# Performance work log

Measured on AMD Instinct MI355X. Metric: run time of the kernel, lower is better.

Reference implementation:

```python
import jax, jax.numpy as jnp
import numpy as np

M, NC, NT, DX = 8, 1024, 512, 3
CHUNK = 512          # chunk_size
N_STEPS = 8          # n_steps (tol=0.0 -> torch early-stop never fires)
LR = 0.1
B1, B2, EPS = 0.9, 0.999, 1e-8
SQRT5 = 5.0 ** 0.5
LOG2PI = float(np.log(2.0 * np.pi))
NOISE_LB = 1e-4      # gpytorch GreaterThan(1e-4) noise constraint


def setup_inputs():
    key = jax.random.key(0)
    k1, k2, k3 = jax.random.split(key, 3)
    return {
        "xc": jax.random.normal(k1, (M, NC, DX), jnp.float32),
        "yc": jax.random.normal(k2, (M, NC, 1), jnp.float32),
        "xt": jax.random.normal(k3, (M, NT, DX), jnp.float32),
    }


def _kernel(x1, x2, ls, outscale):
    # ScaleKernel(MaternKernel(nu=2.5)); ls: [m,1,1], outscale: [m]
    xs1, xs2 = x1 / ls, x2 / ls
    d2 = (jnp.sum(xs1 * xs1, -1)[:, :, None]
          + jnp.sum(xs2 * xs2, -1)[:, None, :]
          - 2.0 * jnp.einsum('mnd,mkd->mnk', xs1, xs2))
    d2 = jnp.clip(d2, 1e-12, None)   # clamp like gpytorch dist for grad safety
    d = jnp.sqrt(d2)
    k = (1.0 + SQRT5 * d + (5.0 / 3.0) * d2) * jnp.exp(-SQRT5 * d)
    return outscale[:, None, None] * k


def _constrained(params):
    ls = jax.nn.softplus(params["raw_ls"])                          # [m,1,1]
    outscale = jax.nn.softplus(params["raw_os"])                    # [m]
    noise = jax.nn.softplus(params["raw_noise"][:, 0]) + NOISE_LB   # [m]
    return ls, outscale, noise


def _nll(params, x, y):
    # sum over tasks of -ExactMarginalLogLikelihood (gpytorch divides by n)
    ls, outscale, noise = _constrained(params)
    n = x.shape[1]
    K = _kernel(x, x, ls, outscale) + noise[:, None, None] * jnp.eye(n, dtype=x.dtype)
    L = jnp.linalg.cholesky(K)
    diff = y - params["const"][:, None]
    alpha = jax.scipy.linalg.cho_solve((L, True), diff[..., None])[..., 0]
    quad = jnp.sum(diff * alpha, -1)
    logdet = 2.0 * jnp.sum(jnp.log(jnp.diagonal(L, axis1=-2, axis2=-1)), -1)
    mll = -0.5 * (quad + logdet + n * LOG2PI) / n
    return jnp.sum(-mll)


def _adam_step(carry, x_sub, y_sub):
    p, m_, v_, t = carry
    g = jax.grad(_nll)(p, x_sub, y_sub)
    t = t + 1.0
    tm = jax.tree_util.tree_map
    m_ = tm(lambda a, gg: B1 * a + (1.0 - B1) * gg, m_, g)
    v_ = tm(lambda a, gg: B2 * a + (1.0 - B2) * gg * gg, v_, g)
    bc1 = 1.0 - B1 ** t
    bc2 = 1.0 - B2 ** t
    p = tm(lambda pp, mm, vv: pp - LR * (mm / bc1) / (jnp.sqrt(vv / bc2) + EPS), p, m_, v_)
    return (p, m_, v_, t)


def _gp_forward(xc, yc, xt):
    y = yc[..., 0]                                    # [m, nc]
    zl = lambda s: jnp.zeros(s, jnp.float32)
    # gpytorch raw params initialize to 0
    params = {"raw_ls": zl((M, 1, 1)), "raw_os": zl((M,)),
              "raw_noise": zl((M, 1)), "const": zl((M,))}
    m_ = jax.tree_util.tree_map(jnp.zeros_like, params)
    v_ = jax.tree_util.tree_map(jnp.zeros_like, params)
    carry = (params, m_, v_, jnp.float32(0.0))
    for i in range(0, NC, CHUNK):                     # 'Expanding' strategy
        end = min(i + CHUNK, NC)
        x_sub, y_sub = xc[:, :end], y[:, :end]
        step = lambda c, _: (_adam_step(c, x_sub, y_sub), None)
        carry, _ = jax.lax.scan(step, carry, None, length=N_STEPS)
    params = carry[0]
    # posterior predictive with trained hypers (train data = full context)
    ls, outscale, noise = _constrained(params)
    Kcc = _kernel(xc, xc, ls, outscale) + noise[:, None, None] * jnp.eye(NC, dtype=xc.dtype)
    L = jnp.linalg.cholesky(Kcc)
    diff = y - params["const"][:, None]
    alpha = jax.scipy.linalg.cho_solve((L, True), diff[..., None])[..., 0]
    Ktc = _kernel(xt, xc, ls, outscale)               # [m, nt, nc]
    mean = params["const"][:, None] + jnp.einsum('mtn,mn->mt', Ktc, alpha)
    v = jax.scipy.linalg.solve_triangular(L, jnp.swapaxes(Ktc, 1, 2), lower=True)  # [m,nc,nt]
    var_f = outscale[:, None] - jnp.sum(v * v, axis=1)  # Matern(0)=1 -> prior diag = outputscale
    var = var_f + noise[:, None]                      # likelihood(f) adds observation noise
    return jnp.stack([mean, var])                     # [2, m, nt]


def reference(xc, yc, xt):
    return _gp_forward(xc, yc, xt)
```

## Files before the change

kernel.cpp:

```cpp
#include <hip/hip_runtime.h>
#include <math.h>

constexpr int MM = 8;
constexpr int NC = 1024;
constexpr int NT = 512;
constexpr int GRID = 512;
constexpr int GPB  = GRID / MM;

constexpr size_t OFF_A     = (size_t)MM * 1024 * 1024;
constexpr size_t OFF_T     = OFF_A * 2;
constexpr size_t OFF_KTC   = OFF_T + (size_t)MM * 512 * 512;
constexpr size_t OFF_ALPHA = OFF_KTC + (size_t)MM * NT * NC;
constexpr size_t OFF_ACC   = OFF_ALPHA + (size_t)MM * 1024;

#define S5 2.2360679775f

struct GBar {
  unsigned slot[GPB][16];
  unsigned gen[16];
  unsigned xcd[GPB][16];
};
__device__ GBar g_bar2[MM];

__device__ __forceinline__ unsigned bar_base(int m) {
  return __hip_atomic_load(&g_bar2[m].gen[0], __ATOMIC_RELAXED, __HIP_MEMORY_SCOPE_AGENT);
}

__device__ __forceinline__ void gbar_full(int m, int gb, unsigned ph) {
  __syncthreads();
  GBar* b = &g_bar2[m];
  const int tid = threadIdx.x;
  if (gb == 0) {
    if (tid >= 1 && tid < GPB) {
      while (__hip_atomic_load(&b->slot[tid][0], __ATOMIC_RELAXED, __HIP_MEMORY_SCOPE_AGENT) < ph)
        __builtin_amdgcn_s_sleep(2);
    }
    __syncthreads();
    if (tid == 0) {
      __threadfence();
      __hip_atomic_store(&b->gen[0], ph, __ATOMIC_RELAXED, __HIP_MEMORY_SCOPE_AGENT);
    }
    __syncthreads();
  } else {
    if (tid == 0) {
      __threadfence();
      __hip_atomic_store(&b->slot[gb][0], ph, __ATOMIC_RELAXED, __HIP_MEMORY_SCOPE_AGENT);
      while (__hip_atomic_load(&b->gen[0], __ATOMIC_RELAXED, __HIP_MEMORY_SCOPE_AGENT) < ph)
        __builtin_amdgcn_s_sleep(8);
      __threadfence();
    }
    __syncthreads();
  }
}

__device__ __forceinline__ void gbar_cheap(int m, int gb, unsigned ph) {
  __syncthreads();
  GBar* b = &g_bar2[m];
  const int tid = threadIdx.x;
  if (gb == 0) {
    if (tid >= 1 && tid < GPB) {
      while (__hip_atomic_load(&b->slot[tid][0], __ATOMIC_RELAXED, __HIP_MEMORY_SCOPE_AGENT) < ph)
        __builtin_amdgcn_s_sleep(2);
    }
    __syncthreads();
    if (tid == 0) {
      asm volatile("s_waitcnt vmcnt(0)" ::: "memory");
      __hip_atomic_store(&b->gen[0], ph, __ATOMIC_RELAXED, __HIP_MEMORY_SCOPE_AGENT);
    }
    __syncthreads();
  } else {
    if (tid == 0) {
      asm volatile("s_waitcnt vmcnt(0)" ::: "memory");
      __hip_atomic_store(&b->slot[gb][0], ph, __ATOMIC_RELAXED, __HIP_MEMORY_SCOPE_AGENT);
      while (__hip_atomic_load(&b->gen[0], __ATOMIC_RELAXED, __HIP_MEMORY_SCOPE_AGENT) < ph)
        __builtin_amdgcn_s_sleep(8);
    }
    __syncthreads();
  }
}

__device__ __forceinline__ void gbar(int m, int gb, unsigned& ph, int cheap) {
  if (cheap) gbar_cheap(m, gb, ph); else gbar_full(m, gb, ph);
  ph++;
}

__device__ __forceinline__ float sigmf(float x) { return 1.0f / (1.0f + expf(-x)); }
__device__ __forceinline__ float softplusf(float x) { return fmaxf(x, 0.0f) + log1pf(expf(-fabsf(x))); }

__device__ __forceinline__ void lt_decode(int x, int& i, int& j) {
  int ii = 0;
  while ((ii + 1) * (ii + 2) / 2 <= x) ++ii;
  i = ii; j = x - ii * (ii + 1) / 2;
}

struct SMem {
  float Ls[64 * 65];
  float Us[64 * 65];
  float Tt[32 * 33];
  float dvec[64];
  float As[16][68];
  float Bs[16][68];
  float xi[64][3];
  float xj[64][3];
  float ai[64];
  float aj[64];
  float red[4][4];
  unsigned bar0;
  int cheap;
};

template <int TA, int TB>
__device__ __forceinline__ void gemm64(const volatile float* __restrict__ A, int lda,
                                       const volatile float* __restrict__ B, int ldb,
                                       int kBeg, int kEnd, float acc[4][4], SMem& sm) {
  int tid = threadIdx.x, tx = tid & 15, ty = tid >> 4;
  float ra[4], rb[4];
  auto ldAB = [&](int k0) {
#pragma unroll
    for (int q = 0; q < 4; ++q) {
      int e = tid + (q << 8);
      if (TA) { int kk = e >> 6, r = e & 63; ra[q] = A[(size_t)(k0 + kk) * lda + r]; }
      else    { int r = e >> 4, kk = e & 15; ra[q] = A[(size_t)r * lda + k0 + kk]; }
      if (TB) { int c = e >> 4, kk = e & 15; rb[q] = B[(size_t)c * ldb + k0 + kk]; }
      else    { int kk = e >> 6, c = e & 63; rb[q] = B[(size_t)(k0 + kk) * ldb + c]; }
    }
  };
  ldAB(kBeg);
  for (int k0 = kBeg; k0 < kEnd; k0 += 16) {
    __syncthreads();
#pragma unroll
    for (int q = 0; q < 4; ++q) {
      int e = tid + (q << 8);
      if (TA) sm.As[e >> 6][e & 63] = ra[q]; else sm.As[e & 15][e >> 4] = ra[q];
      if (TB) sm.Bs[e & 15][e >> 4] = rb[q]; else sm.Bs[e >> 6][e & 63] = rb[q];
    }
    __syncthreads();
    if (k0 + 16 < kEnd) ldAB(k0 + 16);
#pragma unroll
    for (int kk = 0; kk < 16; ++kk) {
      float a[4], b[4];
#pragma unroll
      for (int i = 0; i < 4; ++i) a[i] = sm.As[kk][ty * 4 + i];
#pragma unroll
      for (int j = 0; j < 4; ++j) b[j] = sm.Bs[kk][tx * 4 + j];
#pragma unroll
      for (int i = 0; i < 4; ++i)
#pragma unroll
        for (int j = 0; j < 4; ++j) acc[i][j] = fmaf(a[i], b[j], acc[i][j]);
    }
  }
}

__device__ void factor64(SMem& sm, float* Uout, int ldu) {
  int tid = threadIdx.x;
  int tx = tid & 15, ty = tid >> 4;
  for (int j = 0; j < 63; ++j) {
    float rinv = 1.0f / sm.Ls[j * 65 + j];
    for (int i = j + 1 + ty; i < 64; i += 16) {
      float lij = sm.Ls[i * 65 + j] * rinv;
      for (int c = j + 1 + tx; c <= i; c += 16) sm.Ls[i * 65 + c] -= lij * sm.Ls[c * 65 + j];
    }
    __syncthreads();
  }
  if (tid < 64) sm.dvec[tid] = 1.0f / sqrtf(sm.Ls[tid * 65 + tid]);
  __syncthreads();
  for (int e = tid; e < 4096; e += 256) { int r = e >> 6, c = e & 63; if (c <= r) sm.Ls[r * 65 + c] *= sm.dvec[c]; }
  __syncthreads();
  for (int e = tid; e < 64 * 65; e += 256) sm.Us[e] = 0.0f;
  __syncthreads();
  if (tid < 64) {
    int b = tid >> 5, c0 = tid & 31, base = b * 32, gc = base + c0;
    sm.Us[gc * 65 + gc] = 1.0f / sm.Ls[gc * 65 + gc];
    for (int r = c0 + 1; r < 32; ++r) {
      int gr = base + r;
      float acc = 0.0f;
      for (int l = c0; l < r; ++l) acc += sm.Ls[gr * 65 + base + l] * sm.Us[(base + l) * 65 + gc];
      sm.Us[gr * 65 + gc] = -acc / sm.Ls[gr * 65 + gr];
    }
  }
  __syncthreads();
  for (int e = tid; e < 1024; e += 256) {
    int r = e >> 5, c = e & 31;
    float acc = 0.0f;
    for (int l = c; l < 32; ++l) acc += sm.Ls[(32 + r) * 65 + l] * sm.Us[l * 65 + c];
    sm.Tt[r * 33 + c] = acc;
  }
  __syncthreads();
  for (int e = tid; e < 1024; e += 256) {
    int r = e >> 5, c = e & 31;
    float acc = 0.0f;
    for (int l = 0; l <= r; ++l) acc += sm.Us[(32 + r) * 65 + 32 + l] * sm.Tt[l * 33 + c];
    sm.Us[(32 + r) * 65 + c] = -acc;
  }
  __syncthreads();
  for (int e = tid; e < 4096; e += 256) { int r = e >> 6, c = e & 63; Uout[(size_t)r * ldu + c] = sm.Us[r * 65 + c]; }
}


__device__ void adam_all(const float* __restrict__ yc, const float* __restrict__ ws,
                         int pn, int tstep, int m, int tid, SMem& sm,
                         float praw[4], float pm[4], float pv[4],
                         float& ls, float& os, float& noi, float& cm) {
  const volatile float* al = ws + OFF_ALPHA + (size_t)m * 1024;
  const volatile float* accp = ws + OFF_ACC + m * 8;
  const float* ym = yc + (size_t)m * NC;
  float t4 = 0, t5 = 0, t6 = 0;
  for (int i = tid; i < pn; i += 256) {
    float a = al[i];
    t4 = fmaf(a, a, t4); t5 += a; t6 = fmaf(ym[i] - cm, a, t6);
  }
  for (int off = 32; off; off >>= 1) {
    t4 += __shfl_down(t4, off); t5 += __shfl_down(t5, off); t6 += __shfl_down(t6, off);
  }
  int wid = tid >> 6, lane = tid & 63;
  if (lane == 0) { sm.red[wid][0] = t4; sm.red[wid][1] = t5; sm.red[wid][2] = t6; }
  __syncthreads();
  t4 = sm.red[0][0] + sm.red[1][0] + sm.red[2][0] + sm.red[3][0];
  t5 = sm.red[0][1] + sm.red[1][1] + sm.red[2][1] + sm.red[3][1];
  t6 = sm.red[0][2] + sm.red[1][2] + sm.red[2][2] + sm.red[3][2];
  float T1 = accp[0], T2 = accp[1], t3 = accp[2];
  float fn = (float)pn;
  float g_ls = 0.5f / fn * (T1 - T2);
  float g_os = 0.5f / (fn * os) * (fn - noi * t3 - t6 + noi * t4);
  float g_no = 0.5f / fn * (t3 - t4);
  float g_c = -t5 / fn;
  float gr[4];
  gr[0] = g_ls * sigmf(praw[0]);
  gr[1] = g_os * sigmf(praw[1]);
  gr[2] = g_no * sigmf(praw[2]);
  gr[3] = g_c;
  float bc1 = 1.0f - powf(0.9f, (float)tstep);
  float bc2 = 1.0f - powf(0.999f, (float)tstep);
#pragma unroll
  for (int i = 0; i < 4; ++i) {
    float mv = 0.9f * pm[i] + 0.1f * gr[i];
    float vv = 0.999f * pv[i] + 0.001f * gr[i] * gr[i];
    pm[i] = mv; pv[i] = vv;
    praw[i] = praw[i] - 0.1f * (mv / bc1) / (sqrtf(vv / bc2) + 1e-8f);
  }
  ls = softplusf(praw[0]);
  os = softplusf(praw[1]);
  noi = softplusf(praw[2]) + 1e-4f;
  cm = praw[3];
  __syncthreads();
}

__device__ void d_buildK(const float* __restrict__ xc, float* ws, int n, int job, int m,
                         int tid, SMem& sm, float ls, float os, float noi) {
  const float* xm = xc + (size_t)m * NC * 3;
  float* Km = ws + (size_t)m * 1048576;
  float* Am = ws + OFF_A + (size_t)m * 1048576;
  float il2 = 1.0f / (ls * ls);
  int bi, bj; lt_decode(job, bi, bj);
  if (tid < 64) {
    int r = bi * 64 + tid;
    sm.xi[tid][0] = xm[r * 3 + 0]; sm.xi[tid][1] = xm[r * 3 + 1]; sm.xi[tid][2] = xm[r * 3 + 2];
  } else if (tid < 128) {
    int lr = tid - 64; int r = bj * 64 + lr;
    sm.xj[lr][0] = xm[r * 3 + 0]; sm.xj[lr][1] = xm[r * 3 + 1]; sm.xj[lr][2] = xm[r * 3 + 2];
  }
  __syncthreads();
  if (job == 0) {
    for (int e = tid; e < 4096; e += 256) {
      int r = e >> 6, c = e & 63;
      float d0 = sm.xi[r][0] - sm.xj[c][0], d1 = sm.xi[r][1] - sm.xj[c][1], d2 = sm.xi[r][2] - sm.xj[c][2];
      float r2 = d0 * d0 + d1 * d1 + d2 * d2;
      float z = fmaxf(r2 * il2, 1e-12f);
      float dd = sqrtf(z);
      float kv = os * (1.0f + S5 * dd + (5.0f / 3.0f) * z) * expf(-S5 * dd);
      if (r == c) kv += noi;
      sm.Ls[r * 65 + c] = kv;
    }
    __syncthreads();
    factor64(sm, Am, n);
  } else {
    for (int e = tid; e < 4096; e += 256) {
      int r = e >> 6, c = e & 63;
      float d0 = sm.xi[r][0] - sm.xj[c][0], d1 = sm.xi[r][1] - sm.xj[c][1], d2 = sm.xi[r][2] - sm.xj[c][2];
      float r2 = d0 * d0 + d1 * d1 + d2 * d2;
      float z = fmaxf(r2 * il2, 1e-12f);
      float dd = sqrtf(z);
      float kv = os * (1.0f + S5 * dd + (5.0f / 3.0f) * z) * expf(-S5 * dd);
      if (bi == bj && r == c) kv += noi;
      Km[(size_t)(bi * 64 + r) * n + bj * 64 + c] = kv;
    }
  }
}

__device__ void d_trail(float* ws, int k, int n, int job, int m, int tid, SMem& sm) {
  int tx = tid & 15, ty = tid >> 4;
  float* Km = ws + (size_t)m * 1048576;
  float* Am = ws + OFF_A + (size_t)m * 1048576;
  const volatile float* Linv = Am + (size_t)(k * 64) * n + k * 64;
  int di, dj; lt_decode(job, di, dj);
  int i = k + 1 + di, j = k + 1 + dj;
  float pp[4][4] = {};
  gemm64<0, 1>(Km + (size_t)(i * 64) * n + k * 64, n, Linv, n, 0, 64, pp, sm);
  __syncthreads();
#pragma unroll
  for (int ii = 0; ii < 4; ++ii)
#pragma unroll
    for (int jj = 0; jj < 4; ++jj) sm.Ls[(ty * 4 + ii) * 65 + tx * 4 + jj] = pp[ii][jj];
  if (di == dj) {
    float* P = Am + (size_t)(i * 64) * n + k * 64;
#pragma unroll
    for (int ii = 0; ii < 4; ++ii)
#pragma unroll
      for (int jj = 0; jj < 4; ++jj) P[(size_t)(ty * 4 + ii) * n + tx * 4 + jj] = pp[ii][jj];
  } else {
#pragma unroll
    for (int ii = 0; ii < 4; ++ii)
#pragma unroll
      for (int jj = 0; jj < 4; ++jj) pp[ii][jj] = 0.0f;
    gemm64<0, 1>(Km + (size_t)(j * 64) * n + k * 64, n, Linv, n, 0, 64, pp, sm);
#pragma unroll
    for (int ii = 0; ii < 4; ++ii)
#pragma unroll
      for (int jj = 0; jj < 4; ++jj) sm.Us[(ty * 4 + ii) * 65 + tx * 4 + jj] = pp[ii][jj];
  }
  __syncthreads();
  float acc[4][4] = {};
  {
    const float* Bsrc = (di == dj) ? sm.Ls : sm.Us;
    for (int l = 0; l < 64; ++l) {
      float a[4], b[4];
#pragma unroll
      for (int ii = 0; ii < 4; ++ii) a[ii] = sm.Ls[(ty * 4 + ii) * 65 + l];
#pragma unroll
      for (int jj = 0; jj < 4; ++jj) b[jj] = Bsrc[(tx * 4 + jj) * 65 + l];
#pragma unroll
      for (int ii = 0; ii < 4; ++ii)
#pragma unroll
        for (int jj = 0; jj < 4; ++jj) acc[ii][jj] = fmaf(a[ii], b[jj], acc[ii][jj]);
    }
  }
  float* C = Km + (size_t)(i * 64) * n + j * 64;
  if (job == 0) {
    const volatile float* Cv = C;
    __syncthreads();
#pragma unroll
    for (int ii = 0; ii < 4; ++ii)
#pragma unroll
      for (int jj = 0; jj < 4; ++jj)
        sm.Ls[(ty * 4 + ii) * 65 + tx * 4 + jj] =
            Cv[(size_t)(ty * 4 + ii) * n + tx * 4 + jj] - acc[ii][jj];
    __syncthreads();
    factor64(sm, Am + (size_t)((k + 1) * 64) * n + (k + 1) * 64, n);
  } else {
    const volatile float* Cv = C;
#pragma unroll
    for (int ii = 0; ii < 4; ++ii)
#pragma unroll
      for (int jj = 0; jj < 4; ++jj)
        C[(size_t)(ty * 4 + ii) * n + tx * 4 + jj] =
            Cv[(size_t)(ty * 4 + ii) * n + tx * 4 + jj] - acc[ii][jj];
  }
}

__device__ void d_trinv64(float* ws, int n, int p, int m, int tid, SMem& sm) {
  int tx = tid & 15, ty = tid >> 4;
  float* Am = ws + OFF_A + (size_t)m * 1048576;
  const volatile float* Av = Am;
  int rb = (2 * p + 1) * 64, cb = 2 * p * 64;
  for (int e = tid; e < 4096; e += 256) {
    int r = e >> 6, c = e & 63;
    sm.Ls[r * 65 + c] = Av[(size_t)(rb + r) * n + cb + c];
    sm.Us[r * 65 + c] = Av[(size_t)(cb + r) * n + cb + c];
  }
  __syncthreads();
  float tt[4][4] = {};
  for (int l = 0; l < 64; ++l) {
    float a[4], b[4];
#pragma unroll
    for (int ii = 0; ii < 4; ++ii) a[ii] = sm.Ls[(ty * 4 + ii) * 65 + l];
#pragma unroll
    for (int jj = 0; jj < 4; ++jj) b[jj] = sm.Us[l * 65 + tx * 4 + jj];
#pragma unroll
    for (int ii = 0; ii < 4; ++ii)
#pragma unroll
      for (int jj = 0; jj < 4; ++jj) tt[ii][jj] = fmaf(a[ii], b[jj], tt[ii][jj]);
  }
  __syncthreads();
#pragma unroll
  for (int ii = 0; ii < 4; ++ii)
#pragma unroll
    for (int jj = 0; jj < 4; ++jj) sm.Ls[(ty * 4 + ii) * 65 + tx * 4 + jj] = tt[ii][jj];
  for (int e = tid; e < 4096; e += 256) {
    int r = e >> 6, c = e & 63;
    sm.Us[r * 65 + c] = Av[(size_t)(rb + r) * n + rb + c];
  }
  __syncthreads();
  float oo[4][4] = {};
  for (int l = 0; l < 64; ++l) {
    float a[4], b[4];
#pragma unroll
    for (int ii = 0; ii < 4; ++ii) a[ii] = sm.Us[(ty * 4 + ii) * 65 + l];
#pragma unroll
    for (int jj = 0; jj < 4; ++jj) b[jj] = sm.Ls[l * 65 + tx * 4 + jj];
#pragma unroll
    for (int ii = 0; ii < 4; ++ii)
#pragma unroll
      for (int jj = 0; jj < 4; ++jj) oo[ii][jj] = fmaf(a[ii], b[jj], oo[ii][jj]);
  }
#pragma unroll
  for (int ii = 0; ii < 4; ++ii)
#pragma unroll
    for (int jj = 0; jj < 4; ++jj)
      Am[(size_t)(rb + ty * 4 + ii) * n + cb + tx * 4 + jj] = -oo[ii][jj];
}

__device__ void d_trinvT(float* ws, int s, int n, int job, int m, int tid, SMem& sm) {
  int tx = tid & 15, ty = tid >> 4;
  float* Am = ws + OFF_A + (size_t)m * 1048576;
  float* Tm = ws + OFF_T + (size_t)m * 262144;
  int st = s >> 6;
  int p = job / (st * st), rem = job % (st * st);
  int ti = rem / st, tj = rem % st;
  int base = p * 2 * s;
  float acc[4][4] = {};
  gemm64<0, 0>(Am + (size_t)(base + s + ti * 64) * n + base, n,
               Am + (size_t)base * n + base + tj * 64, n, tj * 64, s, acc, sm);
  float* C = Tm + (size_t)p * s * s + (size_t)(ti * 64) * s + tj * 64;
#pragma unroll
  for (int ii = 0; ii < 4; ++ii)
#pragma unroll
    for (int jj = 0; jj < 4; ++jj) C[(size_t)(ty * 4 + ii) * s + tx * 4 + jj] = acc[ii][jj];
}

__device__ void d_trinvA(float* ws, int s, int n, int job, int m, int tid, SMem& sm) {
  int tx = tid & 15, ty = tid >> 4;
  float* Am = ws + OFF_A + (size_t)m * 1048576;
  const volatile float* Tm = ws + OFF_T + (size_t)m * 262144;
  int st = s >> 6;
  int p = job / (st * st), rem = job % (st * st);
  int ti = rem / st, tj = rem % st;
  int base = p * 2 * s;
  float acc[4][4] = {};
  gemm64<0, 0>(Am + (size_t)(base + s + ti * 64) * n + base + s, n,
               Tm + (size_t)p * s * s + tj * 64, s, 0, (ti + 1) * 64, acc, sm);
  float* C = Am + (size_t)(base + s + ti * 64) * n + base + tj * 64;
#pragma unroll
  for (int ii = 0; ii < 4; ++ii)
#pragma unroll
    for (int jj = 0; jj < 4; ++jj) C[(size_t)(ty * 4 + ii) * n + tx * 4 + jj] = -acc[ii][jj];
}

__device__ void d_syrkAT(const float* __restrict__ yc, const float* __restrict__ xc,
                         float* ws, int n, int job, int m, int tid, SMem& sm,
                         float cm, float ls, float os, bool writeG) {
  int tx = tid & 15, ty = tid >> 4;
  const float* Am = ws + OFF_A + (size_t)m * 1048576;
  float* Gm = ws + (size_t)m * 1048576;
  const float* ym = yc + (size_t)m * NC;
  const float* xm = xc + (size_t)m * NC * 3;
  float* accp = ws + OFF_ACC + m * 8;
  float* al = ws + OFF_ALPHA + (size_t)m * 1024;
  int ib, jb; lt_decode(job, ib, jb);
  if (tid < 64) {
    int r = ib * 64 + tid;
    sm.ai[tid] = ym[r] - cm;
    sm.xi[tid][0] = xm[r * 3 + 0]; sm.xi[tid][1] = xm[r * 3 + 1]; sm.xi[tid][2] = xm[r * 3 + 2];
  } else if (tid < 128) {
    int lr = tid - 64; int r = jb * 64 + lr;
    sm.aj[lr] = ym[r] - cm;
    sm.xj[lr][0] = xm[r * 3 + 0]; sm.xj[lr][1] = xm[r * 3 + 1]; sm.xj[lr][2] = xm[r * 3 + 2];
  }
  float acc[4][4] = {};
  gemm64<1, 0>(Am + ib * 64, n, Am + jb * 64, n, ib * 64, n, acc, sm);
  if (writeG) {
#pragma unroll
    for (int ii = 0; ii < 4; ++ii)
#pragma unroll
      for (int jj = 0; jj < 4; ++jj) {
        int r = ty * 4 + ii, c = tx * 4 + jj;
        Gm[(size_t)(ib * 64 + r) * n + jb * 64 + c] = acc[ii][jj];
        if (ib != jb) Gm[(size_t)(jb * 64 + c) * n + ib * 64 + r] = acc[ii][jj];
      }
  }
  if (ib == jb && tx == ty) {
    atomicAdd(&accp[2], acc[0][0] + acc[1][1] + acc[2][2] + acc[3][3]);
  }
  float rowp[4];
#pragma unroll
  for (int i = 0; i < 4; ++i) {
    float s = 0.0f;
#pragma unroll
    for (int j = 0; j < 4; ++j) s = fmaf(acc[i][j], sm.aj[tx * 4 + j], s);
    rowp[i] = s;
  }
  float colp[4];
  if (ib != jb) {
#pragma unroll
    for (int j = 0; j < 4; ++j) {
      float s = 0.0f;
#pragma unroll
      for (int i = 0; i < 4; ++i) s = fmaf(acc[i][j], sm.ai[ty * 4 + i], s);
      colp[j] = s;
    }
  }
  float il2 = 1.0f / (ls * ls);
  float c53 = (5.0f / 3.0f) * os / ls;
  float a1 = 0.0f;
#pragma unroll
  for (int ii = 0; ii < 4; ++ii) {
    int r = ty * 4 + ii;
#pragma unroll
    for (int jj = 0; jj < 4; ++jj) {
      int c = tx * 4 + jj;
      float d0 = sm.xi[r][0] - sm.xj[c][0], d1 = sm.xi[r][1] - sm.xj[c][1], d2 = sm.xi[r][2] - sm.xj[c][2];
      float r2 = d0 * d0 + d1 * d1 + d2 * d2;
      float z = fmaxf(r2 * il2, 1e-12f);
      float dd = sqrtf(z);
      float Cv = c53 * z * (1.0f + S5 * dd) * expf(-S5 * dd);
      a1 = fmaf(acc[ii][jj], Cv, a1);
    }
  }
  a1 *= (ib == jb) ? 1.0f : 2.0f;
  for (int off = 32; off; off >>= 1) a1 += __shfl_down(a1, off);
  int wid = tid >> 6, lane = tid & 63;
  if (lane == 0) sm.red[wid][0] = a1;
  __syncthreads();
  if (tid == 0)
    atomicAdd(&accp[0], sm.red[0][0] + sm.red[1][0] + sm.red[2][0] + sm.red[3][0]);
  float* redA = &sm.As[0][0];
  float* redB = &sm.Bs[0][0];
#pragma unroll
  for (int i = 0; i < 4; ++i) redA[(ty * 4 + i) * 16 + tx] = rowp[i];
  if (ib != jb) {
#pragma unroll
    for (int j = 0; j < 4; ++j) redB[(tx * 4 + j) * 16 + ty] = colp[j];
  }
  __syncthreads();
  if (tid < 64) {
    float s = 0.0f;
#pragma unroll
    for (int q = 0; q < 16; ++q) s += redA[tid * 16 + q];
    atomicAdd(&al[ib * 64 + tid], s);
    if (ib != jb) {
      float s2 = 0.0f;
#pragma unroll
      for (int q = 0; q < 16; ++q) s2 += redB[tid * 16 + q];
      atomicAdd(&al[jb * 64 + tid], s2);
    }
  }
}

__device__ void d_reduce2(const float* __restrict__ xc, float* ws, int n, int job, int m,
                          int tid, SMem& sm, float ls, float os) {
  const float* xm = xc + (size_t)m * NC * 3;
  const volatile float* al = ws + OFF_ALPHA + (size_t)m * 1024;
  float* accp = ws + OFF_ACC + m * 8;
  float il2 = 1.0f / (ls * ls);
  float c53 = (5.0f / 3.0f) * os / ls;
  int bi, bj; lt_decode(job, bi, bj);
  float w = (bi == bj) ? 1.0f : 2.0f;
  if (tid < 64) {
    int r = bi * 64 + tid;
    sm.xi[tid][0] = xm[r * 3 + 0]; sm.xi[tid][1] = xm[r * 3 + 1]; sm.xi[tid][2] = xm[r * 3 + 2];
    sm.ai[tid] = al[r];
  } else if (tid < 128) {
    int lr = tid - 64; int r = bj * 64 + lr;
    sm.xj[lr][0] = xm[r * 3 + 0]; sm.xj[lr][1] = xm[r * 3 + 1]; sm.xj[lr][2] = xm[r * 3 + 2];
    sm.aj[lr] = al[r];
  }
  __syncthreads();
  float a2 = 0.0f;
  for (int e = tid; e < 4096; e += 256) {
    int r = e >> 6, c = e & 63;
    float d0 = sm.xi[r][0] - sm.xj[c][0], d1 = sm.xi[r][1] - sm.xj[c][1], d2 = sm.xi[r][2] - sm.xj[c][2];
    float r2 = d0 * d0 + d1 * d1 + d2 * d2;
    float z = fmaxf(r2 * il2, 1e-12f);
    float dd = sqrtf(z);
    float Cv = c53 * z * (1.0f + S5 * dd) * expf(-S5 * dd);
    a2 = fmaf(sm.ai[r] * sm.aj[c], Cv, a2);
  }
  a2 *= w;
  for (int off = 32; off; off >>= 1) a2 += __shfl_down(a2, off);
  int wid = tid >> 6, lane = tid & 63;
  if (lane == 0) sm.red[wid][1] = a2;
  __syncthreads();
  if (tid == 0) {
    atomicAdd(&accp[1], sm.red[0][1] + sm.red[1][1] + sm.red[2][1] + sm.red[3][1]);
  }
}

__device__ void d_buildKtc(const float* __restrict__ xt, const float* __restrict__ xc,
                           float* ws, int job, int m, int tid, SMem& sm, float ls, float os) {
  const float* xtm = xt + (size_t)m * NT * 3;
  const float* xm = xc + (size_t)m * NC * 3;
  float* Kt = ws + OFF_KTC + (size_t)m * NT * NC;
  float* Tm = ws + OFF_T + (size_t)m * 262144;
  float il2 = 1.0f / (ls * ls);
  if (job < 2) {
    int z = job * 256 + tid;
    Tm[z] = 0.0f; Tm[NT + z] = 0.0f;
  }
  int ti = job >> 4, tj = job & 15;
  if (tid < 64) {
    int r = ti * 64 + tid;
    sm.xi[tid][0] = xtm[r * 3 + 0]; sm.xi[tid][1] = xtm[r * 3 + 1]; sm.xi[tid][2] = xtm[r * 3 + 2];
  } else if (tid < 128) {
    int lr = tid - 64; int r = tj * 64 + lr;
    sm.xj[lr][0] = xm[r * 3 + 0]; sm.xj[lr][1] = xm[r * 3 + 1]; sm.xj[lr][2] = xm[r * 3 + 2];
  }
  __syncthreads();
  for (int e = tid; e < 4096; e += 256) {
    int r = e >> 6, c = e & 63;
    float d0 = sm.xi[r][0] - sm.xj[c][0], d1 = sm.xi[r][1] - sm.xj[c][1], d2 = sm.xi[r][2] - sm.xj[c][2];
    float r2 = d0 * d0 + d1 * d1 + d2 * d2;
    float z = fmaxf(r2 * il2, 1e-12f);
    float dd = sqrtf(z);
    float kv = os * (1.0f + S5 * dd + (5.0f / 3.0f) * z) * expf(-S5 * dd);
    Kt[(size_t)(ti * 64 + r) * NC + tj * 64 + c] = kv;
  }
}

__device__ void d_predW(float* ws, int job, int m, int tid, SMem& sm) {
  int tx = tid & 15, ty = tid >> 4;
  const volatile float* Kt = ws + OFF_KTC + (size_t)m * NT * NC;
  const volatile float* Gm = ws + (size_t)m * 1048576;
  const volatile float* al = ws + OFF_ALPHA + (size_t)m * 1024;
  float* S1 = ws + OFF_T + (size_t)m * 262144;
  float* S2 = S1 + NT;
  int ti = job >> 4, tj = job & 15;
  if (tid < 64) sm.aj[tid] = al[tj * 64 + tid];
  float acc[4][4] = {};
  gemm64<0, 0>(Kt + (size_t)(ti * 64) * NC, NC, Gm + tj * 64, 1024, 0, 1024, acc, sm);
  float s1p[4], s2p[4];
#pragma unroll
  for (int i = 0; i < 4; ++i) {
    float a1 = 0.0f, a2 = 0.0f;
    const volatile float* kr = Kt + (size_t)(ti * 64 + ty * 4 + i) * NC + tj * 64;
#pragma unroll
    for (int j = 0; j < 4; ++j) {
      float kv = kr[tx * 4 + j];
      a1 = fmaf(kv, sm.aj[tx * 4 + j], a1);
      a2 = fmaf(kv, acc[i][j], a2);
    }
    s1p[i] = a1; s2p[i] = a2;
  }
  __syncthreads();
  float* redA = &sm.As[0][0];
  float* redB = &sm.Bs[0][0];
#pragma unroll
  for (int i = 0; i < 4; ++i) {
    redA[(ty * 4 + i) * 16 + tx] = s1p[i];
    redB[(ty * 4 + i) * 16 + tx] = s2p[i];
  }
  __syncthreads();
  if (tid < 64) {
    float a1 = 0.0f, a2 = 0.0f;
#pragma unroll
    for (int q = 0; q < 16; ++q) { a1 += redA[tid * 16 + q]; a2 += redB[tid * 16 + q]; }
    atomicAdd(&S1[ti * 64 + tid], a1);
    atomicAdd(&S2[ti * 64 + tid], a2);
  }
}

__global__ __launch_bounds__(256, 2) void k_gp(const float* __restrict__ xc,
                                               const float* __restrict__ yc,
                                               const float* __restrict__ xt,
                                               float* ws, float* out) {
  __shared__ SMem sm;
  const int bid = blockIdx.x;
  const int m  = bid % MM;
  const int gb = bid / MM;
  const int tid = threadIdx.x;

  if (tid == 0) sm.bar0 = bar_base(m);
  __syncthreads();
  unsigned ph = sm.bar0 + 1;

  if (tid == 0) {
    unsigned x;
    asm volatile("s_getreg_b32 %0, hwreg(HW_REG_XCC_ID)" : "=s"(x));
    __hip_atomic_store(&g_bar2[m].xcd[gb][0], x, __ATOMIC_RELAXED, __HIP_MEMORY_SCOPE_AGENT);
  }
  gbar_full(m, gb, ph);
  ph++;
  if (tid < GPB) {
    unsigned v = __hip_atomic_load(&g_bar2[m].xcd[tid][0], __ATOMIC_RELAXED, __HIP_MEMORY_SCOPE_AGENT);
    unsigned v0 = __shfl(v, 0, 64);
    unsigned long long bal = __ballot(v == v0);
    if (tid == 0) sm.cheap = (bal == ~0ull) ? 1 : 0;
  }
  __syncthreads();
  const int cheap = sm.cheap;

  float praw[4] = {0.f, 0.f, 0.f, 0.f};
  float pm[4]   = {0.f, 0.f, 0.f, 0.f};
  float pv[4]   = {0.f, 0.f, 0.f, 0.f};
  float ls = 0.69314718056f, os = 0.69314718056f;
  float noi = 0.69314718056f + 1e-4f, cm = 0.0f;

  for (int step = 0; step < 17; ++step) {
    const int n = step < 8 ? 512 : 1024;
    const int nb = n >> 6;
    const bool lastStep = (step == 16);

    if (step > 0) {
      adam_all(yc, ws, step <= 8 ? 512 : 1024, step, m, tid, sm,
               praw, pm, pv, ls, os, noi, cm);
    }
    {
      const int tot = nb * (nb + 1) / 2;
      if (gb == 0) {
        __syncthreads();
        d_buildK(xc, ws, n, 0, m, tid, sm, ls, os, noi);
      } else {
        for (int q = gb; q < tot; q += GPB - 1) {
          __syncthreads();
          d_buildK(xc, ws, n, q, m, tid, sm, ls, os, noi);
        }
      }
      gbar(m, gb, ph, cheap);
    }

    for (int k = 0; k <= nb - 2; ++k) {
      const int t = nb - 1 - k;
      const int tot = t * (t + 1) / 2;
      if (gb == 0) {
        if (k == 0) {
          float* al = ws + OFF_ALPHA + (size_t)m * 1024;
          for (int z = tid; z < 1024; z += 256) al[z] = 0.0f;
          if (tid < 8) ws[OFF_ACC + m * 8 + tid] = 0.0f;
        }
        __syncthreads();
        d_trail(ws, k, n, 0, m, tid, sm);
      } else {
        for (int q = gb; q < tot; q += GPB - 1) {
          __syncthreads();
          d_trail(ws, k, n, q, m, tid, sm);
        }
        if ((k & 1) && gb == GPB - 1) {
          __syncthreads();
          d_trinv64(ws, n, k >> 1, m, tid, sm);
        }
      }
      gbar(m, gb, ph, cheap);
    }

    for (int s = 128; s < n; s <<= 1) {
      const int st = s >> 6;
      const int np = n / (2 * s);
      const int tot = np * st * st;
      for (int q = gb; q < tot; q += GPB) {
        __syncthreads();
        d_trinvT(ws, s, n, q, m, tid, sm);
      }
      if (s == 128 && gb == GPB - 1) {
        __syncthreads();
        d_trinv64(ws, n, nb / 2 - 1, m, tid, sm);
      }
      gbar(m, gb, ph, cheap);
      for (int q = gb; q < tot; q += GPB) {
        __syncthreads();
        d_trinvA(ws, s, n, q, m, tid, sm);
      }
      gbar(m, gb, ph, cheap);
    }

    {
      const int tot = nb * (nb + 1) / 2;
      for (int q = gb; q < tot; q += GPB) {
        __syncthreads();
        d_syrkAT(yc, xc, ws, n, q, m, tid, sm, cm, ls, os, lastStep);
      }
      gbar(m, gb, ph, cheap);
    }

    if (step < 16) {
      const int tot = nb * (nb + 1) / 2;
      for (int q = gb; q < tot; q += GPB) {
        __syncthreads();
        d_reduce2(xc, ws, n, q, m, tid, sm, ls, os);
      }
      gbar(m, gb, ph, cheap);
    }
  }

  {
    for (int q = gb; q < 128; q += GPB) {
      __syncthreads();
      d_buildKtc(xt, xc, ws, q, m, tid, sm, ls, os);
    }
    gbar(m, gb, ph, cheap);
    for (int q = gb; q < 128; q += GPB) {
      __syncthreads();
      d_predW(ws, q, m, tid, sm);
    }
    gbar(m, gb, ph, cheap);
    const volatile float* S1 = ws + OFF_T + (size_t)m * 262144;
    const volatile float* S2 = S1 + NT;
    for (int t = gb * 256 + tid; t < NT; t += GPB * 256) {
      out[(size_t)m * NT + t] = cm + S1[t];
      out[(size_t)MM * NT + (size_t)m * NT + t] = os + noi - S2[t];
    }
  }
}

extern "C" void kernel_launch(void* const* d_in, const int* in_sizes, int n_in,
                              void* d_out, int out_size, void* d_ws, size_t ws_size,
                              hipStream_t stream) {
  const float* xc = (const float*)d_in[0];
  const float* yc = (const float*)d_in[1];
  const float* xt = (const float*)d_in[2];
  float* out = (float*)d_out;
  float* ws = (float*)d_ws;

  hipLaunchKernelGGL(k_gp, dim3(GRID), dim3(256), 0, stream, xc, yc, xt, ws, out);

  (void)in_sizes; (void)n_in; (void)out_size; (void)ws_size;
}
```

Measured before the change: 21.46 ms.

## Map each task's block group to one XCD and use cheap intra-XCD barriers

Blocks now claim a rank within their hardware XCD at startup, so each of the 8 tasks runs entirely on one XCD with a variable group size. This lets every per-task barrier use the cheap waitcnt-only path instead of full device fences and lets shared data stay in one XCD's L2. It also raises wave priority for the critical-path block 0 work and serpentine-orders the syrk tile assignment for load balance. The risk is that XCD block counts are uneven, or that correctness now depends on the claim protocol and on all blocks being co-resident.

```diff
diff --git a/kernel.cpp b/kernel.cpp
--- a/kernel.cpp
+++ b/kernel.cpp
@@ -5,7 +5,7 @@
 constexpr int NC = 1024;
 constexpr int NT = 512;
 constexpr int GRID = 512;
-constexpr int GPB  = GRID / MM;
+constexpr int GPB_MAX = 96;
 
 constexpr size_t OFF_A     = (size_t)MM * 1024 * 1024;
 constexpr size_t OFF_T     = OFF_A * 2;
@@ -16,49 +16,20 @@
 #define S5 2.2360679775f
 
 struct GBar {
-  unsigned slot[GPB][16];
+  unsigned slot[GPB_MAX][16];
   unsigned gen[16];
-  unsigned xcd[GPB][16];
 };
 __device__ GBar g_bar2[MM];
-
-__device__ __forceinline__ unsigned bar_base(int m) {
-  return __hip_atomic_load(&g_bar2[m].gen[0], __ATOMIC_RELAXED, __HIP_MEMORY_SCOPE_AGENT);
-}
-
-__device__ __forceinline__ void gbar_full(int m, int gb, unsigned ph) {
+__device__ unsigned g_claim[MM][GPB_MAX][16];
+__device__ unsigned g_gcnt = 0;
+__device__ unsigned g_ggen = 0;
+
+__device__ __forceinline__ void gbar(int m, int gb, int gpbn, unsigned& ph) {
   __syncthreads();
   GBar* b = &g_bar2[m];
   const int tid = threadIdx.x;
   if (gb == 0) {
-    if (tid >= 1 && tid < GPB) {
-      while (__hip_atomic_load(&b->slot[tid][0], __ATOMIC_RELAXED, __HIP_MEMORY_SCOPE_AGENT) < ph)
-        __builtin_amdgcn_s_sleep(2);
-    }
-    __syncthreads();
-    if (tid == 0) {
-      __threadfence();
-      __hip_atomic_store(&b->gen[0], ph, __ATOMIC_RELAXED, __HIP_MEMORY_SCOPE_AGENT);
-    }
-    __syncthreads();
-  } else {
-    if (tid == 0) {
-      __threadfence();
-      __hip_atomic_store(&b->slot[gb][0], ph, __ATOMIC_RELAXED, __HIP_MEMORY_SCOPE_AGENT);
-      while (__hip_atomic_load(&b->gen[0], __ATOMIC_RELAXED, __HIP_MEMORY_SCOPE_AGENT) < ph)
-        __builtin_amdgcn_s_sleep(8);
-      __threadfence();
-    }
-    __syncthreads();
-  }
-}
-
-__device__ __forceinline__ void gbar_cheap(int m, int gb, unsigned ph) {
-  __syncthreads();
-  GBar* b = &g_bar2[m];
-  const int tid = threadIdx.x;
-  if (gb == 0) {
-    if (tid >= 1 && tid < GPB) {
+    if (tid >= 1 && tid < gpbn) {
       while (__hip_atomic_load(&b->slot[tid][0], __ATOMIC_RELAXED, __HIP_MEMORY_SCOPE_AGENT) < ph)
         __builtin_amdgcn_s_sleep(2);
     }
@@ -73,14 +44,10 @@
       asm volatile("s_waitcnt vmcnt(0)" ::: "memory");
       __hip_atomic_store(&b->slot[gb][0], ph, __ATOMIC_RELAXED, __HIP_MEMORY_SCOPE_AGENT);
       while (__hip_atomic_load(&b->gen[0], __ATOMIC_RELAXED, __HIP_MEMORY_SCOPE_AGENT) < ph)
-        __builtin_amdgcn_s_sleep(8);
-    }
-    __syncthreads();
-  }
-}
-
-__device__ __forceinline__ void gbar(int m, int gb, unsigned& ph, int cheap) {
-  if (cheap) gbar_cheap(m, gb, ph); else gbar_full(m, gb, ph);
+        __builtin_amdgcn_s_sleep(4);
+    }
+    __syncthreads();
+  }
   ph++;
 }
 
@@ -106,7 +73,7 @@
   float aj[64];
   float red[4][4];
   unsigned bar0;
-  int cheap;
+  int m, rank, gpbn;
 };
 
 template <int TA, int TB>
@@ -662,30 +629,38 @@
                                                const float* __restrict__ xt,
                                                float* ws, float* out) {
   __shared__ SMem sm;
-  const int bid = blockIdx.x;
-  const int m  = bid % MM;
-  const int gb = bid / MM;
   const int tid = threadIdx.x;
 
-  if (tid == 0) sm.bar0 = bar_base(m);
-  __syncthreads();
-  unsigned ph = sm.bar0 + 1;
-
   if (tid == 0) {
+    unsigned G0 = __hip_atomic_load(&g_ggen, __ATOMIC_RELAXED, __HIP_MEMORY_SCOPE_AGENT);
+    unsigned E = G0 + 1u;
     unsigned x;
     asm volatile("s_getreg_b32 %0, hwreg(HW_REG_XCC_ID)" : "=s"(x));
-    __hip_atomic_store(&g_bar2[m].xcd[gb][0], x, __ATOMIC_RELAXED, __HIP_MEMORY_SCOPE_AGENT);
-  }
-  gbar_full(m, gb, ph);
-  ph++;
-  if (tid < GPB) {
-    unsigned v = __hip_atomic_load(&g_bar2[m].xcd[tid][0], __ATOMIC_RELAXED, __HIP_MEMORY_SCOPE_AGENT);
-    unsigned v0 = __shfl(v, 0, 64);
-    unsigned long long bal = __ballot(v == v0);
-    if (tid == 0) sm.cheap = (bal == ~0ull) ? 1 : 0;
-  }
-  __syncthreads();
-  const int cheap = sm.cheap;
+    x &= 7u;
+    int r = 0;
+    for (int i = 0; i < GPB_MAX; ++i) {
+      unsigned old = __hip_atomic_exchange(&g_claim[x][i][0], E, __ATOMIC_RELAXED, __HIP_MEMORY_SCOPE_AGENT);
+      if (old != E) { r = i; break; }
+    }
+    __threadfence();
+    unsigned a = __hip_atomic_fetch_add(&g_gcnt, 1u, __ATOMIC_ACQ_REL, __HIP_MEMORY_SCOPE_AGENT);
+    if (a + 1u == (unsigned)GRID) {
+      __hip_atomic_store(&g_gcnt, 0u, __ATOMIC_RELAXED, __HIP_MEMORY_SCOPE_AGENT);
+      __hip_atomic_store(&g_ggen, E, __ATOMIC_RELEASE, __HIP_MEMORY_SCOPE_AGENT);
+    } else {
+      while (__hip_atomic_load(&g_ggen, __ATOMIC_ACQUIRE, __HIP_MEMORY_SCOPE_AGENT) < E)
+        __builtin_amdgcn_s_sleep(16);
+    }
+    __threadfence();
+    int n = 0;
+    for (int i = 0; i < GPB_MAX; ++i)
+      n += (__hip_atomic_load(&g_claim[x][i][0], __ATOMIC_RELAXED, __HIP_MEMORY_SCOPE_AGENT) == E);
+    sm.m = (int)x; sm.rank = r; sm.gpbn = n;
+    sm.bar0 = __hip_atomic_load(&g_bar2[x].gen[0], __ATOMIC_RELAXED, __HIP_MEMORY_SCOPE_AGENT);
+  }
+  __syncthreads();
+  const int m = sm.m, gb = sm.rank, gpbn = sm.gpbn;
+  unsigned ph = sm.bar0 + 1;
 
   float praw[4] = {0.f, 0.f, 0.f, 0.f};
   float pm[4]   = {0.f, 0.f, 0.f, 0.f};
@@ -706,14 +681,16 @@
       const int tot = nb * (nb + 1) / 2;
       if (gb == 0) {
         __syncthreads();
+        __builtin_amdgcn_s_setprio(1);
         d_buildK(xc, ws, n, 0, m, tid, sm, ls, os, noi);
+        __builtin_amdgcn_s_setprio(0);
       } else {
-        for (int q = gb; q < tot; q += GPB - 1) {
+        for (int q = gb; q < tot; q += gpbn - 1) {
           __syncthreads();
           d_buildK(xc, ws, n, q, m, tid, sm, ls, os, noi);
         }
       }
-      gbar(m, gb, ph, cheap);
+      gbar(m, gb, gpbn, ph);
     }
 
     for (int k = 0; k <= nb - 2; ++k) {
@@ -726,73 +703,80 @@
           if (tid < 8) ws[OFF_ACC + m * 8 + tid] = 0.0f;
         }
         __syncthreads();
+        __builtin_amdgcn_s_setprio(1);
         d_trail(ws, k, n, 0, m, tid, sm);
+        __builtin_amdgcn_s_setprio(0);
       } else {
-        for (int q = gb; q < tot; q += GPB - 1) {
+        for (int q = gb; q < tot; q += gpbn - 1) {
           __syncthreads();
           d_trail(ws, k, n, q, m, tid, sm);
         }
-        if ((k & 1) && gb == GPB - 1) {
+        if ((k & 1) && gb == gpbn - 1) {
           __syncthreads();
           d_trinv64(ws, n, k >> 1, m, tid, sm);
         }
       }
-      gbar(m, gb, ph, cheap);
+      gbar(m, gb, gpbn, ph);
     }
 
     for (int s = 128; s < n; s <<= 1) {
       const int st = s >> 6;
       const int np = n / (2 * s);
       const int tot = np * st * st;
-      for (int q = gb; q < tot; q += GPB) {
+      for (int q = gb; q < tot; q += gpbn) {
         __syncthreads();
         d_trinvT(ws, s, n, q, m, tid, sm);
       }
-      if (s == 128 && gb == GPB - 1) {
+      if (s == 128 && gb == gpbn - 1) {
         __syncthreads();
         d_trinv64(ws, n, nb / 2 - 1, m, tid, sm);
       }
-      gbar(m, gb, ph, cheap);
-      for (int q = gb; q < tot; q += GPB) {
+      gbar(m, gb, gpbn, ph);
+      for (int q = gb; q < tot; q += gpbn) {
         __syncthreads();
         d_trinvA(ws, s, n, q, m, tid, sm);
       }
-      gbar(m, gb, ph, cheap);
+      gbar(m, gb, gpbn, ph);
     }
 
     {
       const int tot = nb * (nb + 1) / 2;
-      for (int q = gb; q < tot; q += GPB) {
-        __syncthreads();
-        d_syrkAT(yc, xc, ws, n, q, m, tid, sm, cm, ls, os, lastStep);
+      for (int t = 0;; ++t) {
+        int base = t * gpbn;
+        if (base >= tot) break;
+        int q = base + ((t & 1) ? (gpbn - 1 - gb) : gb);
+        if (q < tot) {
+          __syncthreads();
+          d_syrkAT(yc, xc, ws, n, q, m, tid, sm, cm, ls, os, lastStep);
+        }
       }
-      gbar(m, gb, ph, cheap);
+      gbar(m, gb, gpbn, ph);
     }
 
     if (step < 16) {
       const int tot = nb * (nb + 1) / 2;
-      for (int q = gb; q < tot; q += GPB) {
+      for (int q = gb; q < tot; q += gpbn) {
         __syncthreads();
         d_reduce2(xc, ws, n, q, m, tid, sm, ls, os);
       }
-      gbar(m, gb, ph, cheap);
+      gbar(m, gb, gpbn, ph);
     }
   }
 
   {
-    for (int q = gb; q < 128; q += GPB) {
+    for (int q = gb; q < 128; q += gpbn) {
       __syncthreads();
       d_buildKtc(xt, xc, ws, q, m, tid, sm, ls, os);
     }
-    gbar(m, gb, ph, cheap);
-    for (int q = gb; q < 128; q += GPB) {
+    gbar(m, gb, gpbn, ph);
+    for (int q = gb; q < 128; q += gpbn) {
       __syncthreads();
       d_predW(ws, q, m, tid, sm);
     }
-    gbar(m, gb, ph, cheap);
+    gbar(m, gb, gpbn, ph);
     const volatile float* S1 = ws + OFF_T + (size_t)m * 262144;
     const volatile float* S2 = S1 + NT;
-    for (int t = gb * 256 + tid; t < NT; t += GPB * 256) {
+    for (int t = gb * 256 + tid; t < NT; t += gpbn * 256) {
       out[(size_t)m * NT + t] = cm + S1[t];
       out[(size_t)MM * NT + (size_t)m * NT + t] = os + noi - S2[t];
     }
```

New measurement: 21.06 ms. Within noise of the previous version (-1.9%).
